# Optimization experiments

Measured on AMD Instinct MI355X. Metric: run time of the kernel, lower is better.

## Reference

```python
import jax, jax.numpy as jnp
import numpy as np
import math

# ---- config (matches init_kwargs / Mamba defaults) ----
B_SZ = 16
IMG = 224
PATCH = 16
D_MODEL = 384
DEPTH = 24
D_INNER = 2 * D_MODEL          # expand=2
D_STATE = 16
D_CONV = 4
DT_RANK = math.ceil(D_MODEL / D_STATE)
N_CLASSES = 1000
L_TOK = (IMG // PATCH) ** 2     # 196

C_CURV = 0.5
SQRT_C = math.sqrt(C_CURV)
MAX_NORM = 0.95 / SQRT_C

# ---- StablePoincareBall ops ----
def _norm(x):
    return jnp.sqrt(jnp.sum(x * x, axis=-1, keepdims=True) + 1e-15)

def expmap0(u):
    n = jnp.clip(_norm(u), 1e-8, 5.0)
    res = jnp.tanh(SQRT_C * n) / SQRT_C * (u / n)
    rn = _norm(res)
    scale = jnp.where(rn > MAX_NORM, MAX_NORM / rn, jnp.ones_like(rn))
    return res * scale

def logmap0(y):
    n = jnp.clip(_norm(y), 1e-8, MAX_NORM)
    return jnp.arctanh(jnp.minimum(SQRT_C * n, 0.95)) / SQRT_C * (y / n)

def mobius_add(a, b):
    xy = jnp.sum(a * b, -1, keepdims=True)
    x2 = jnp.sum(a * a, -1, keepdims=True)
    y2 = jnp.sum(b * b, -1, keepdims=True)
    num = (1 + 2 * C_CURV * xy + C_CURV * y2) * a + (1 - C_CURV * x2) * b
    den = 1 + 2 * C_CURV * xy + (C_CURV ** 2) * x2 * y2
    return num / jnp.maximum(den, 1e-15)

def mobius_matvec(M, x):
    xn = jnp.maximum(_norm(x), 1e-8)
    mx = x @ M.T
    mxn = jnp.maximum(_norm(mx), 1e-8)
    t = jnp.tanh(mxn / xn * jnp.arctanh(jnp.minimum(SQRT_C * xn, 1.0 - 1e-5)))
    return t * mx / (mxn * SQRT_C)

def hyp_layernorm(x, gamma, beta, eps=1e-5):
    t = logmap0(x)
    mean = t.mean(-1, keepdims=True)
    # torch .std() is unbiased (ddof=1)
    var = jnp.sum((t - mean) ** 2, -1, keepdims=True) / (t.shape[-1] - 1)
    tn = (t - mean) / (jnp.sqrt(var) + eps)
    return expmap0(tn * gamma + beta)

def silu(x):
    return x * jax.nn.sigmoid(x)

# ---- Mamba selective scan (recompute dA per step; carry only h) ----
def selective_scan(u, dt, A, Bm, Cm):
    # u, dt: (B,L,Din); A: (Din,N); Bm, Cm: (B,L,N)
    def step(h, inp):
        dt_t, B_t, C_t, u_t = inp              # (B,Din),(B,N),(B,N),(B,Din)
        dA = jnp.exp(dt_t[..., None] * A)      # (B,Din,N)
        h = dA * h + dt_t[..., None] * B_t[:, None, :] * u_t[..., None]
        y = jnp.sum(h * C_t[:, None, :], -1)   # (B,Din)
        return h, y
    h0 = jnp.zeros((u.shape[0], u.shape[2], A.shape[1]), u.dtype)
    _, ys = jax.lax.scan(step, h0, (dt.transpose(1, 0, 2), Bm.transpose(1, 0, 2),
                                    Cm.transpose(1, 0, 2), u.transpose(1, 0, 2)))
    return ys.transpose(1, 0, 2)               # (B,L,Din)

def mamba_mixer(x, in_w, cw, cb, xp_w, dt_w, dt_b, A_log, Dp, out_w):
    xz = x @ in_w.T                            # (B,L,2*Din)
    xc, z = xz[..., :D_INNER], xz[..., D_INNER:]
    xt = xc.transpose(0, 2, 1)                 # (B,Din,L)
    xpad = jnp.pad(xt, ((0, 0), (0, 0), (D_CONV - 1, 0)))
    L = xt.shape[-1]
    conv = sum(cw[:, k][None, :, None] * xpad[:, :, k:k + L] for k in range(D_CONV))
    conv = conv + cb[None, :, None]
    u = silu(conv.transpose(0, 2, 1))          # (B,L,Din)
    dbl = u @ xp_w.T                           # (B,L,dt_rank+2N)
    dt_r = dbl[..., :DT_RANK]
    Bm = dbl[..., DT_RANK:DT_RANK + D_STATE]
    Cm = dbl[..., DT_RANK + D_STATE:]
    dt = jax.nn.softplus(dt_r @ dt_w.T + dt_b)
    A = -jnp.exp(A_log)
    y = selective_scan(u, dt, A, Bm, Cm) + Dp * u
    y = y * silu(z)
    return y @ out_w.T


def setup_inputs() -> dict:
    key = jax.random.key(0)
    ks = jax.random.split(key, 24)
    f32 = jnp.float32
    inp = {}
    inp['x'] = jax.random.normal(ks[0], (B_SZ, 3, IMG, IMG), f32)
    inp['patch_w'] = jax.random.normal(ks[1], (D_MODEL, 3, PATCH, PATCH), f32) * 0.02
    inp['patch_b'] = jax.random.normal(ks[2], (D_MODEL,), f32) * 0.005
    inp['hyp_w'] = jax.random.normal(ks[3], (D_MODEL, D_MODEL), f32) * (1.0 / math.sqrt(D_MODEL))
    inp['hyp_b'] = jax.random.normal(ks[4], (D_MODEL,), f32) * 0.01
    inp['pe_gamma'] = jnp.ones((D_MODEL,), f32)
    inp['pe_beta'] = jnp.zeros((D_MODEL,), f32)
    inp['pos_embed'] = jax.random.normal(ks[5], (1, L_TOK, D_MODEL), f32) * 0.02
    inp['in_proj_w'] = jax.random.normal(ks[6], (DEPTH, 2 * D_INNER, D_MODEL), f32) * 0.02
    inp['conv_w'] = jax.random.normal(ks[7], (DEPTH, D_INNER, D_CONV), f32) * 0.1
    inp['conv_b'] = jnp.zeros((DEPTH, D_INNER), f32)
    inp['x_proj_w'] = jax.random.normal(ks[8], (DEPTH, DT_RANK + 2 * D_STATE, D_INNER), f32) * 0.02
    inp['dt_proj_w'] = jax.random.normal(ks[9], (DEPTH, D_INNER, DT_RANK), f32) * (1.0 / math.sqrt(DT_RANK))
    inp['dt_proj_b'] = jnp.log(jnp.expm1(jnp.full((DEPTH, D_INNER), 0.01, f32)))  # dt init ~0.01
    inp['A_log'] = jnp.tile(jnp.log(jnp.arange(1, D_STATE + 1, dtype=f32))[None, None, :], (DEPTH, D_INNER, 1))
    inp['Dp'] = jnp.ones((DEPTH, D_INNER), f32)
    inp['out_proj_w'] = jax.random.normal(ks[10], (DEPTH, D_MODEL, D_INNER), f32) * (0.02 / math.sqrt(DEPTH))
    inp['gamma'] = jnp.ones((DEPTH, D_MODEL), f32)
    inp['beta'] = jnp.zeros((DEPTH, D_MODEL), f32)
    inp['gamma_f'] = jnp.ones((D_MODEL,), f32)
    inp['beta_f'] = jnp.zeros((D_MODEL,), f32)
    inp['prototypes'] = expmap0(jax.random.normal(ks[11], (N_CLASSES, D_MODEL), f32) * 0.1)
    return inp


def reference(x, patch_w, patch_b, hyp_w, hyp_b, pe_gamma, pe_beta, pos_embed,
              in_proj_w, conv_w, conv_b, x_proj_w, dt_proj_w, dt_proj_b,
              A_log, Dp, out_proj_w, gamma, beta, gamma_f, beta_f, prototypes):
    # patch embed conv
    feat = jax.lax.conv_general_dilated(x, patch_w, (PATCH, PATCH), 'VALID',
                                        dimension_numbers=('NCHW', 'OIHW', 'NCHW'))
    feat = feat + patch_b[None, :, None, None]
    B, D, Hp, Wp = feat.shape
    tokens = feat.reshape(B, D, Hp * Wp).transpose(0, 2, 1)   # (B,L,D)
    h = expmap0(tokens)
    h = mobius_add(mobius_matvec(hyp_w, h), hyp_b)
    h = hyp_layernorm(h, pe_gamma, pe_beta)
    h = expmap0(logmap0(h) + pos_embed)                        # tangent-space pos add
    hidden, residual = h, None
    for i in range(DEPTH):
        residual = hidden if residual is None else hidden + residual
        hn = hyp_layernorm(residual, gamma[i], beta[i])
        hidden = mamba_mixer(hn, in_proj_w[i], conv_w[i], conv_b[i], x_proj_w[i],
                             dt_proj_w[i], dt_proj_b[i], A_log[i], Dp[i], out_proj_w[i])
    residual = hidden + residual
    hf = hyp_layernorm(residual, gamma_f, beta_f)
    pooled = expmap0(logmap0(hf).mean(axis=1))                 # tangent mean pool
    # hyperbolic distance head: logits = -dist(x, prototypes)
    diff = mobius_add(-pooled[:, None, :], prototypes[None])
    dn = jnp.minimum(SQRT_C * _norm(diff)[..., 0], 1.0 - 1e-5)
    return -(2.0 / SQRT_C) * jnp.arctanh(dn)                   # (B, num_classes)
```

## Files before the change

### kernel.cpp

```cpp
#include <hip/hip_runtime.h>
#include <hip/hip_bf16.h>
#include <math.h>

#define D_MODEL 384
#define D_INNER 768
#define D_STATE 16
#define DT_RANK 24
#define NXP 56
#define LTOK 196
#define BSZ 16
#define NROW 3136
#define NDEPTH 24
#define NCLS 1000

constexpr float kSqrtC   = 0.70710678118654752440f;
constexpr float kMaxNorm = 0.95f / 0.70710678118654752440f;

typedef unsigned short u16;
typedef short  bf16x8 __attribute__((ext_vector_type(8)));
typedef u16    u16x8  __attribute__((ext_vector_type(8)));
typedef float  f32x4  __attribute__((ext_vector_type(4)));

__device__ __forceinline__ float clampf(float x, float lo, float hi) {
  return fminf(fmaxf(x, lo), hi);
}

__device__ __forceinline__ u16 f2bf(float f) {
  union { float f; unsigned u; } v; v.f = f;
  return (u16)((v.u + 0x7FFFu + ((v.u >> 16) & 1u)) >> 16);
}
__device__ __forceinline__ float bf2f(u16 s) {
  union { unsigned u; float f; } v; v.u = ((unsigned)s) << 16;
  return v.f;
}

__device__ __forceinline__ void gload16(const u16* g, u16* l) {
  __builtin_amdgcn_global_load_lds(
      (const __attribute__((address_space(1))) unsigned int*)g,
      (__attribute__((address_space(3))) unsigned int*)l, 16, 0, 0);
}

__device__ __forceinline__ float fsig(float x) {
  return __fdividef(1.f, 1.f + __expf(-x));
}
__device__ __forceinline__ float fsilu(float x) { return x * fsig(x); }
__device__ __forceinline__ float fsoftplus(float x) {
  return (x > 20.f) ? x : __logf(1.f + __expf(x));
}
__device__ __forceinline__ float ftanh(float x) {
  float e = __expf(2.f * x);
  return __fdividef(e - 1.f, e + 1.f);
}
__device__ __forceinline__ float fatanh(float x) {
  return 0.5f * __logf(__fdividef(1.f + x, 1.f - x));
}

__device__ __forceinline__ float waveSum(float v) {
#pragma unroll
  for (int o = 1; o < 64; o <<= 1) v += __shfl_xor(v, o, 64);
  return v;
}

__device__ __forceinline__ float blockSum128(float v, float* sm) {
#pragma unroll
  for (int o = 32; o > 0; o >>= 1) v += __shfl_down(v, o, 64);
  __syncthreads();
  if ((threadIdx.x & 63) == 0) sm[threadIdx.x >> 6] = v;
  __syncthreads();
  return sm[0] + sm[1];
}

__global__ __launch_bounds__(256) void k_cvt(const float* __restrict__ s,
                                             u16* __restrict__ d, int n4) {
  int i = blockIdx.x * 256 + threadIdx.x;
  if (i >= n4) return;
  float4 v = ((const float4*)s)[i];
  short4 o = {(short)f2bf(v.x), (short)f2bf(v.y), (short)f2bf(v.z),
              (short)f2bf(v.w)};
  *(short4*)&d[(size_t)i * 4] = o;
}

__global__ __launch_bounds__(256) void k_im2col(const float* __restrict__ x,
                                                u16* __restrict__ P) {
  size_t idx = (size_t)blockIdx.x * 256 + threadIdx.x;
  if (idx >= (size_t)NROW * 768) return;
  int k = (int)(idx % 768);
  int r = (int)(idx / 768);
  int b = r / LTOK, t = r % LTOK;
  int hp = t / 14, wp = t % 14;
  int c = k / 256, rem = k % 256, i = rem / 16, j = rem % 16;
  P[idx] = f2bf(
      x[(((size_t)(b * 3 + c) * 224) + hp * 16 + i) * 224 + wp * 16 + j]);
}

__global__ __launch_bounds__(256) void k_gemm_bb(
    const u16* __restrict__ A, const u16* __restrict__ W,
    const float* __restrict__ bias, void* __restrict__ Cn,
    void* __restrict__ Ct, int K, int lda, int ldc, int ldct, int Nv, int act,
    int obf, int obf_t) {
  __shared__ u16 As[64 * 64];
  __shared__ u16 Ws[64 * 64];
  const int tid = threadIdx.x;
  const int m0 = blockIdx.x * 64;
  const int n0 = blockIdx.y * 64;
  const int lane = tid & 63;
  const int w = tid >> 6;
  const int wm = w & 1, wn = w >> 1;
  const int lm = lane & 15;
  const int quad = lane >> 4;
  const int r8 = lane >> 3;
  const int t8 = lane & 7;
  const int gsg = t8 ^ r8;
  const int s = lm & 7;

  f32x4 acc[2][2];
#pragma unroll
  for (int i = 0; i < 2; i++)
#pragma unroll
    for (int j = 0; j < 2; j++) acc[i][j] = (f32x4){0.f, 0.f, 0.f, 0.f};

  for (int k0 = 0; k0 < K; k0 += 64) {
    __syncthreads();
#pragma unroll
    for (int cc = 0; cc < 2; cc++) {
      const int c = 2 * w + cc;
      const int row = c * 8 + r8;
      gload16(A + (size_t)(m0 + row) * lda + k0 + gsg * 8,
              (u16*)As + (size_t)c * 512);
      gload16(W + (size_t)(n0 + row) * K + k0 + gsg * 8,
              (u16*)Ws + (size_t)c * 512);
    }
    __syncthreads();
#pragma unroll
    for (int h = 0; h < 2; h++) {
      const int col = (((h << 2) + quad) ^ s) << 3;
      bf16x8 af[2], bfr[2];
#pragma unroll
      for (int i = 0; i < 2; i++) {
        af[i]  = *(bf16x8*)&As[(wm * 32 + i * 16 + lm) * 64 + col];
        bfr[i] = *(bf16x8*)&Ws[(wn * 32 + i * 16 + lm) * 64 + col];
      }
#pragma unroll
      for (int i = 0; i < 2; i++)
#pragma unroll
        for (int j = 0; j < 2; j++)
          acc[i][j] = __builtin_amdgcn_mfma_f32_16x16x32_bf16(
              af[i], bfr[j], acc[i][j], 0, 0, 0);
    }
  }
#pragma unroll
  for (int i = 0; i < 2; i++) {
#pragma unroll
    for (int j = 0; j < 2; j++) {
      int cg = n0 + wn * 32 + j * 16 + lm;
      if (cg >= Nv) continue;
      float bj = bias ? bias[cg] : 0.f;
      float o[4];
      int rgb = m0 + wm * 32 + i * 16 + quad * 4;
#pragma unroll
      for (int reg = 0; reg < 4; reg++) {
        float v = acc[i][j][reg] + bj;
        if (act == 1) v = fsoftplus(v);
        else if (act == 2 && cg >= 768) v = fsilu(v);
        o[reg] = v;
      }
      if (Cn) {
#pragma unroll
        for (int reg = 0; reg < 4; reg++) {
          if (obf) ((u16*)Cn)[(size_t)(rgb + reg) * ldc + cg] = f2bf(o[reg]);
          else ((float*)Cn)[(size_t)(rgb + reg) * ldc + cg] = o[reg];
        }
      }
      if (Ct) {
        if (obf_t) {
          short4 o4 = {(short)f2bf(o[0]), (short)f2bf(o[1]), (short)f2bf(o[2]),
                       (short)f2bf(o[3])};
          *(short4*)&((u16*)Ct)[(size_t)cg * ldct + rgb] = o4;
        } else {
          float4 o4 = {o[0], o[1], o[2], o[3]};
          *(float4*)&((float*)Ct)[(size_t)cg * ldct + rgb] = o4;
        }
      }
    }
  }
}

__global__ __launch_bounds__(256) void k_gemm_n128(
    const u16* __restrict__ A, const u16* __restrict__ W,
    const float* __restrict__ bias, void* __restrict__ Cn, int K, int lda,
    int ldc, int act, int obf) {
  __shared__ u16 As[64 * 64];
  __shared__ u16 Ws[128 * 64];
  const int tid = threadIdx.x;
  const int m0 = blockIdx.x * 64;
  const int n0 = blockIdx.y * 128;
  const int lane = tid & 63;
  const int w = tid >> 6;
  const int lm = lane & 15;
  const int quad = lane >> 4;
  const int r8 = lane >> 3;
  const int t8 = lane & 7;
  const int gsg = t8 ^ r8;
  const int s = lm & 7;

  f32x4 acc[4][2];
#pragma unroll
  for (int i = 0; i < 4; i++)
#pragma unroll
    for (int j = 0; j < 2; j++) acc[i][j] = (f32x4){0.f, 0.f, 0.f, 0.f};

  for (int k0 = 0; k0 < K; k0 += 64) {
    __syncthreads();
#pragma unroll
    for (int cc = 0; cc < 2; cc++) {
      const int c = 2 * w + cc;
      gload16(A + (size_t)(m0 + c * 8 + r8) * lda + k0 + gsg * 8,
              (u16*)As + (size_t)c * 512);
    }
#pragma unroll
    for (int cc = 0; cc < 4; cc++) {
      const int c = 4 * w + cc;
      gload16(W + (size_t)(n0 + c * 8 + r8) * K + k0 + gsg * 8,
              (u16*)Ws + (size_t)c * 512);
    }
    __syncthreads();
#pragma unroll
    for (int h = 0; h < 2; h++) {
      const int col = (((h << 2) + quad) ^ s) << 3;
      bf16x8 af[4], bfr[2];
#pragma unroll
      for (int i = 0; i < 4; i++)
        af[i] = *(bf16x8*)&As[(i * 16 + lm) * 64 + col];
#pragma unroll
      for (int j = 0; j < 2; j++)
        bfr[j] = *(bf16x8*)&Ws[(w * 32 + j * 16 + lm) * 64 + col];
#pragma unroll
      for (int i = 0; i < 4; i++)
#pragma unroll
        for (int j = 0; j < 2; j++)
          acc[i][j] = __builtin_amdgcn_mfma_f32_16x16x32_bf16(
              af[i], bfr[j], acc[i][j], 0, 0, 0);
    }
  }
#pragma unroll
  for (int i = 0; i < 4; i++) {
#pragma unroll
    for (int j = 0; j < 2; j++) {
      int cg = n0 + w * 32 + j * 16 + lm;
      float bj = bias ? bias[cg] : 0.f;
      int rgb = m0 + i * 16 + quad * 4;
#pragma unroll
      for (int reg = 0; reg < 4; reg++) {
        float v = acc[i][j][reg] + bj;
        if (act == 1) v = fsoftplus(v);
        else if (act == 2 && cg >= 768) v = fsilu(v);
        if (obf) ((u16*)Cn)[(size_t)(rgb + reg) * ldc + cg] = f2bf(v);
        else ((float*)Cn)[(size_t)(rgb + reg) * ldc + cg] = v;
      }
    }
  }
}

__global__ __launch_bounds__(128) void k_stem_a(const float* __restrict__ tok,
                                                u16* __restrict__ hb,
                                                float* __restrict__ xn) {
  __shared__ float sm[2];
  const int r = blockIdx.x, tid = threadIdx.x;
  float v[3];
#pragma unroll
  for (int j = 0; j < 3; j++) v[j] = tok[(size_t)r * D_MODEL + tid + j * 128];
  float s = blockSum128(v[0] * v[0] + v[1] * v[1] + v[2] * v[2], sm);
  float n = sqrtf(s + 1e-15f);
  float nc = clampf(n, 1e-8f, 5.f);
  float ke = tanhf(kSqrtC * nc) / (kSqrtC * nc);
  float rn = sqrtf(ke * ke * s + 1e-15f);
  float sc = rn > kMaxNorm ? kMaxNorm / rn : 1.f;
  float kk = ke * sc;
#pragma unroll
  for (int j = 0; j < 3; j++)
    hb[(size_t)r * D_MODEL + tid + j * 128] = f2bf(kk * v[j]);
  if (tid == 0) xn[r] = fmaxf(sqrtf(kk * kk * s + 1e-15f), 1e-8f);
}

__global__ __launch_bounds__(128) void k_stem_b(
    const float* __restrict__ mx, const float* __restrict__ xn,
    const float* __restrict__ hyp_b, const float* __restrict__ pe_g,
    const float* __restrict__ pe_b, const float* __restrict__ pos,
    float* __restrict__ outh) {
  __shared__ float sm[2];
  const int r = blockIdx.x, tid = threadIdx.x;
  const int t = r % LTOK;
  float mv[3], bv[3];
  int dd[3];
#pragma unroll
  for (int j = 0; j < 3; j++) {
    dd[j] = tid + j * 128;
    mv[j] = mx[(size_t)r * D_MODEL + dd[j]];
    bv[j] = hyp_b[dd[j]];
  }
  float smx = blockSum128(mv[0] * mv[0] + mv[1] * mv[1] + mv[2] * mv[2], sm);
  float mxn = fmaxf(sqrtf(smx + 1e-15f), 1e-8f);
  float xnv = xn[r];
  float tt = tanhf(mxn / xnv * atanhf(fminf(kSqrtC * xnv, 1.f - 1e-5f)));
  float kres = tt / (mxn * kSqrtC);
  float res[3];
#pragma unroll
  for (int j = 0; j < 3; j++) res[j] = kres * mv[j];
  float xy = blockSum128(res[0] * bv[0] + res[1] * bv[1] + res[2] * bv[2], sm);
  float y2 = blockSum128(bv[0] * bv[0] + bv[1] * bv[1] + bv[2] * bv[2], sm);
  float x2 = kres * kres * smx;
  float al = 1.f + xy + 0.5f * y2;
  float be = 1.f - 0.5f * x2;
  float den = fmaxf(1.f + xy + 0.25f * x2 * y2, 1e-15f);
  float h1[3];
#pragma unroll
  for (int j = 0; j < 3; j++) h1[j] = (al * res[j] + be * bv[j]) / den;
  float s1 = blockSum128(h1[0] * h1[0] + h1[1] * h1[1] + h1[2] * h1[2], sm);
  float n1 = sqrtf(s1 + 1e-15f);
  float nc1 = clampf(n1, 1e-8f, kMaxNorm);
  float kl = atanhf(fminf(kSqrtC * nc1, 0.95f)) / (kSqrtC * nc1);
  float tl[3];
#pragma unroll
  for (int j = 0; j < 3; j++) tl[j] = kl * h1[j];
  float mean = blockSum128(tl[0] + tl[1] + tl[2], sm) * (1.f / 384.f);
  float dv = 0.f;
#pragma unroll
  for (int j = 0; j < 3; j++) { float d = tl[j] - mean; dv += d * d; }
  float var = blockSum128(dv, sm) * (1.f / 383.f);
  float inv = 1.f / (sqrtf(var) + 1e-5f);
  float g[3];
#pragma unroll
  for (int j = 0; j < 3; j++)
    g[j] = (tl[j] - mean) * inv * pe_g[dd[j]] + pe_b[dd[j]];
  float sg = blockSum128(g[0] * g[0] + g[1] * g[1] + g[2] * g[2], sm);
  float ng = sqrtf(sg + 1e-15f);
  float nc2 = clampf(ng, 1e-8f, 5.f);
  float ke = tanhf(kSqrtC * nc2) / (kSqrtC * nc2);
  float rn = sqrtf(ke * ke * sg + 1e-15f);
  float sc = rn > kMaxNorm ? kMaxNorm / rn : 1.f;
  float kk = ke * sc;
  float s2 = kk * kk * sg;
  float n3 = sqrtf(s2 + 1e-15f);
  float nc3 = clampf(n3, 1e-8f, kMaxNorm);
  float kl2 = atanhf(fminf(kSqrtC * nc3, 0.95f)) / (kSqrtC * nc3);
  float v[3];
#pragma unroll
  for (int j = 0; j < 3; j++)
    v[j] = kl2 * kk * g[j] + pos[(size_t)t * D_MODEL + dd[j]];
  float sv = blockSum128(v[0] * v[0] + v[1] * v[1] + v[2] * v[2], sm);
  float nv = sqrtf(sv + 1e-15f);
  float nc4 = clampf(nv, 1e-8f, 5.f);
  float ke2 = tanhf(kSqrtC * nc4) / (kSqrtC * nc4);
  float rn2 = sqrtf(ke2 * ke2 * sv + 1e-15f);
  float sc2 = rn2 > kMaxNorm ? kMaxNorm / rn2 : 1.f;
#pragma unroll
  for (int j = 0; j < 3; j++)
    outh[(size_t)r * D_MODEL + dd[j]] = ke2 * sc2 * v[j];
}

__global__ __launch_bounds__(256) void k_resln(
    const float* __restrict__ hid, const float* __restrict__ res_in,
    float* __restrict__ res_out, const float* __restrict__ g_,
    const float* __restrict__ b_, u16* __restrict__ out_bf,
    float* __restrict__ out_f, int first, int out_logmap) {
  const int lane = threadIdx.x & 63;
  const int r = blockIdx.x * 4 + (threadIdx.x >> 6);
  float v[6];
  int dd[6];
#pragma unroll
  for (int j = 0; j < 6; j++) {
    dd[j] = lane + j * 64;
    size_t idx = (size_t)r * D_MODEL + dd[j];
    v[j] = hid[idx] + (first ? 0.f : res_in[idx]);
    res_out[idx] = v[j];
  }
  float ss = 0.f;
#pragma unroll
  for (int j = 0; j < 6; j++) ss += v[j] * v[j];
  float s = waveSum(ss);
  float n = sqrtf(s + 1e-15f);
  float nc = clampf(n, 1e-8f, kMaxNorm);
  float kl = fatanh(fminf(kSqrtC * nc, 0.95f)) / (kSqrtC * nc);
  float t[6];
  float ts = 0.f;
#pragma unroll
  for (int j = 0; j < 6; j++) { t[j] = kl * v[j]; ts += t[j]; }
  float mean = waveSum(ts) * (1.f / 384.f);
  float dv = 0.f;
#pragma unroll
  for (int j = 0; j < 6; j++) { float d = t[j] - mean; dv += d * d; }
  float var = waveSum(dv) * (1.f / 383.f);
  float inv = 1.f / (sqrtf(var) + 1e-5f);
  float g[6];
  float gs = 0.f;
#pragma unroll
  for (int j = 0; j < 6; j++) {
    g[j] = (t[j] - mean) * inv * g_[dd[j]] + b_[dd[j]];
    gs += g[j] * g[j];
  }
  float sg = waveSum(gs);
  float ng = sqrtf(sg + 1e-15f);
  float nc2 = clampf(ng, 1e-8f, 5.f);
  float ke = ftanh(kSqrtC * nc2) / (kSqrtC * nc2);
  float rn = sqrtf(ke * ke * sg + 1e-15f);
  float sc = rn > kMaxNorm ? kMaxNorm / rn : 1.f;
  float kk = ke * sc;
  if (!out_logmap) {
#pragma unroll
    for (int j = 0; j < 6; j++)
      out_bf[(size_t)r * D_MODEL + dd[j]] = f2bf(kk * g[j]);
  } else {
    float s2 = kk * kk * sg;
    float n3 = sqrtf(s2 + 1e-15f);
    float nc3 = clampf(n3, 1e-8f, kMaxNorm);
    float kl2 = fatanh(fminf(kSqrtC * nc3, 0.95f)) / (kSqrtC * nc3);
#pragma unroll
    for (int j = 0; j < 6; j++)
      out_f[(size_t)r * D_MODEL + dd[j]] = kl2 * kk * g[j];
  }
}

__global__ __launch_bounds__(256) void k_convt(const u16* __restrict__ xz,
                                               const float* __restrict__ cw,
                                               const float* __restrict__ cb,
                                               u16* __restrict__ ut,
                                               u16* __restrict__ un) {
  __shared__ u16 sx[52][68];
  __shared__ u16 su2[49][68];
  const int d0 = blockIdx.x * 64;
  const int l0 = blockIdx.y * 49;
  const int b = blockIdx.z;
  const int t = threadIdx.x;
#pragma unroll
  for (int i = 0; i < 4; i++) {
    int idx = t + i * 256;
    if (idx < 832) {
      int row = idx >> 4, seg = idx & 15;
      int l = l0 - 3 + row;
      short4 v = {0, 0, 0, 0};
      if (l >= 0) {
        const u16* p = xz + (size_t)(b * LTOK + l) * (2 * D_INNER) + d0 + seg * 4;
        v = *(const short4*)p;
      }
      *(short4*)&sx[row][seg * 4] = v;
    }
  }
  __syncthreads();
  const int dl = t & 63, lg = t >> 6;
  const int d = d0 + dl;
  const float c0 = cw[d * 4], c1 = cw[d * 4 + 1], c2 = cw[d * 4 + 2],
              c3 = cw[d * 4 + 3];
  const float bb = cb[d];
  for (int l = lg; l < 49; l += 4) {
    float acc = bb;
    acc = fmaf(c0, bf2f(sx[l + 0][dl]), acc);
    acc = fmaf(c1, bf2f(sx[l + 1][dl]), acc);
    acc = fmaf(c2, bf2f(sx[l + 2][dl]), acc);
    acc = fmaf(c3, bf2f(sx[l + 3][dl]), acc);
    su2[l][dl] = f2bf(fsilu(acc));
  }
  __syncthreads();
#pragma unroll
  for (int i = 0; i < 13; i++) {
    int idx = t + i * 256;
    if (idx < 3136) {
      int d_ = idx / 49, l_ = idx % 49;
      ut[(size_t)(d0 + d_) * NROW + b * LTOK + l0 + l_] = su2[l_][d_];
    }
  }
#pragma unroll
  for (int i = 0; i < 13; i++) {
    int idx = t + i * 256;
    if (idx < 3136) {
      int l_ = idx >> 6, d_ = idx & 63;
      un[(size_t)(b * LTOK + l0 + l_) * D_INNER + d0 + d_] = su2[l_][d_];
    }
  }
}

__global__ __launch_bounds__(256) void k_pscan(
    const u16* __restrict__ ut, const float* __restrict__ dblt,
    const float* __restrict__ dt_w, const float* __restrict__ dt_bias,
    const float* __restrict__ A_log, const float* __restrict__ Dp,
    const u16* __restrict__ xz, u16* __restrict__ yf) {
  __shared__ float sdt[4][196];
  __shared__ float su[4][196];
  __shared__ float sprod[16][197];
  const int d0 = blockIdx.x * 4, b = blockIdx.y;
  const int t = threadIdx.x;
  const size_t col0 = (size_t)b * LTOK;
  short4 zq = {0, 0, 0, 0};
  if (t < 196) {
    float r[DT_RANK];
#pragma unroll
    for (int k = 0; k < DT_RANK; k++)
      r[k] = dblt[(size_t)k * NROW + col0 + t];
#pragma unroll
    for (int g = 0; g < 4; g++) {
      const int d = d0 + g;
      float acc = dt_bias[d];
#pragma unroll
      for (int k = 0; k < DT_RANK; k++)
        acc = fmaf(r[k], dt_w[d * DT_RANK + k], acc);
      sdt[g][t] = fsoftplus(acc);
      su[g][t] = bf2f(ut[(size_t)d * NROW + col0 + t]);
    }
    zq = *(const short4*)&xz[(col0 + t) * (2 * D_INNER) + D_INNER + d0];
  }
  const int c = t & 15, n = t >> 4;
  const bool act = c < 14;
  float Breg[14], Creg[14];
  if (act) {
    const float2* Bp =
        (const float2*)(dblt + (size_t)(DT_RANK + n) * NROW + col0 + c * 14);
    const float2* Cp = (const float2*)(
        dblt + (size_t)(DT_RANK + D_STATE + n) * NROW + col0 + c * 14);
#pragma unroll
    for (int j = 0; j < 7; j++) {
      float2 bv = Bp[j], cv = Cp[j];
      Breg[2 * j] = bv.x; Breg[2 * j + 1] = bv.y;
      Creg[2 * j] = cv.x; Creg[2 * j + 1] = cv.y;
    }
  }
  __syncthreads();
  u16 og[4];
  const u16 zz[4] = {(u16)zq.x, (u16)zq.y, (u16)zq.z, (u16)zq.w};
#pragma unroll
  for (int g = 0; g < 4; g++) {
    const int d = d0 + g;
    const float a = -__expf(A_log[(size_t)d * D_STATE + n]);
    float dA[14], hh[14];
    float A = 1.f, Bc = 0.f;
    if (act) {
      float h = 0.f, p = 1.f;
#pragma unroll
      for (int j = 0; j < 14; j++) {
        int l = c * 14 + j;
        float dtv = sdt[g][l];
        float e = __expf(dtv * a);
        h = fmaf(e, h, dtv * Breg[j] * su[g][l]);
        dA[j] = e;
        hh[j] = h;
        p *= e;
      }
      A = p;
      Bc = h;
    }
#pragma unroll
    for (int off = 1; off < 16; off <<= 1) {
      float pA = __shfl_up(A, off, 16);
      float pB = __shfl_up(Bc, off, 16);
      if (c >= off) {
        Bc = fmaf(A, pB, Bc);
        A *= pA;
      }
    }
    float h0 = __shfl_up(Bc, 1, 16);
    if (c == 0) h0 = 0.f;
    if (act) {
      float p = 1.f;
#pragma unroll
      for (int j = 0; j < 14; j++) {
        p *= dA[j];
        sprod[n][c * 14 + j] = fmaf(p, h0, hh[j]) * Creg[j];
      }
    }
    __syncthreads();
    if (t < 196) {
      float y = 0.f;
#pragma unroll
      for (int nn = 0; nn < 16; nn++) y += sprod[nn][t];
      float yv = bf2f(f2bf(fmaf(Dp[d], su[g][t], y)));
      og[g] = f2bf(yv * bf2f(zz[g]));
    }
    __syncthreads();
  }
  if (t < 196) {
    short4 o4 = {(short)og[0], (short)og[1], (short)og[2], (short)og[3]};
    *(short4*)&yf[(col0 + t) * D_INNER + d0] = o4;
  }
}

__global__ __launch_bounds__(128) void k_pool1(const float* __restrict__ tl,
                                               float* __restrict__ partial) {
  const int b = blockIdx.x, g = blockIdx.y, tid = threadIdx.x;
  float m[3] = {0.f, 0.f, 0.f};
  for (int l = g * 14; l < (g + 1) * 14; l++) {
    size_t row = ((size_t)b * LTOK + l) * D_MODEL;
#pragma unroll
    for (int j = 0; j < 3; j++) m[j] += tl[row + tid + j * 128];
  }
#pragma unroll
  for (int j = 0; j < 3; j++)
    partial[((size_t)b * 14 + g) * D_MODEL + tid + j * 128] = m[j];
}

__global__ __launch_bounds__(128) void k_pool2(const float* __restrict__ partial,
                                               float* __restrict__ pooled,
                                               float* __restrict__ x2v) {
  __shared__ float sm[2];
  const int b = blockIdx.x, tid = threadIdx.x;
  float m[3] = {0.f, 0.f, 0.f};
  for (int g = 0; g < 14; g++) {
    size_t row = ((size_t)b * 14 + g) * D_MODEL;
#pragma unroll
    for (int j = 0; j < 3; j++) m[j] += partial[row + tid + j * 128];
  }
#pragma unroll
  for (int j = 0; j < 3; j++) m[j] *= (1.f / (float)LTOK);
  float s = blockSum128(m[0] * m[0] + m[1] * m[1] + m[2] * m[2], sm);
  float n = sqrtf(s + 1e-15f);
  float nc = clampf(n, 1e-8f, 5.f);
  float ke = tanhf(kSqrtC * nc) / (kSqrtC * nc);
  float rn = sqrtf(ke * ke * s + 1e-15f);
  float sc = rn > kMaxNorm ? kMaxNorm / rn : 1.f;
  float kk = ke * sc;
  float p[3];
#pragma unroll
  for (int j = 0; j < 3; j++) {
    p[j] = kk * m[j];
    pooled[(size_t)b * D_MODEL + tid + j * 128] = p[j];
  }
  float s2 = blockSum128(p[0] * p[0] + p[1] * p[1] + p[2] * p[2], sm);
  if (tid == 0) x2v[b] = s2;
}

__global__ __launch_bounds__(256) void k_head(const float* __restrict__ pooled,
                                              const float* __restrict__ protos,
                                              const float* __restrict__ x2v,
                                              float* __restrict__ out) {
  __shared__ float sp[D_MODEL];
  const int b = blockIdx.y;
  const int c = blockIdx.x * 256 + threadIdx.x;
  for (int j = threadIdx.x; j < D_MODEL; j += 256)
    sp[j] = pooled[(size_t)b * D_MODEL + j];
  __syncthreads();
  if (c >= NCLS) return;
  const float* pr = protos + (size_t)c * D_MODEL;
  float dotv = 0.f, y2 = 0.f;
  for (int k = 0; k < D_MODEL; k++) {
    float w = pr[k];
    dotv += sp[k] * w;
    y2 += w * w;
  }
  float x2 = x2v[b];
  float xy = -dotv;
  float al = 1.f + xy + 0.5f * y2;
  float be = 1.f - 0.5f * x2;
  float num2 = al * al * x2 + 2.f * al * be * xy + be * be * y2;
  float den = fmaxf(1.f + xy + 0.25f * x2 * y2, 1e-15f);
  float r2 = num2 / (den * den) + 1e-15f;
  float dn = fminf(kSqrtC * sqrtf(r2), 1.f - 1e-5f);
  out[(size_t)b * NCLS + c] = -(2.f / kSqrtC) * atanhf(dn);
}

extern "C" void kernel_launch(void* const* d_in, const int* in_sizes, int n_in,
                              void* d_out, int out_size, void* d_ws,
                              size_t ws_size, hipStream_t stream) {
  const float* x        = (const float*)d_in[0];
  const float* patch_w  = (const float*)d_in[1];
  const float* patch_b  = (const float*)d_in[2];
  const float* hyp_w    = (const float*)d_in[3];
  const float* hyp_b    = (const float*)d_in[4];
  const float* pe_gamma = (const float*)d_in[5];
  const float* pe_beta  = (const float*)d_in[6];
  const float* pos      = (const float*)d_in[7];
  const float* in_w     = (const float*)d_in[8];
  const float* conv_w   = (const float*)d_in[9];
  const float* conv_b   = (const float*)d_in[10];
  const float* xp_w     = (const float*)d_in[11];
  const float* dt_w     = (const float*)d_in[12];
  const float* dt_bias  = (const float*)d_in[13];
  const float* A_log    = (const float*)d_in[14];
  const float* Dp       = (const float*)d_in[15];
  const float* out_w    = (const float*)d_in[16];
  const float* gamma    = (const float*)d_in[17];
  const float* beta     = (const float*)d_in[18];
  const float* gamma_f  = (const float*)d_in[19];
  const float* beta_f   = (const float*)d_in[20];
  const float* protos   = (const float*)d_in[21];
  float* out = (float*)d_out;

  char* cur = (char*)d_ws;
  auto alloc = [&](size_t bytes) {
    char* p = cur;
    cur += (bytes + 255) & ~(size_t)255;
    return (void*)p;
  };
  float* hidden  = (float*)alloc((size_t)NROW * D_MODEL * 4);
  float* resid   = (float*)alloc((size_t)NROW * D_MODEL * 4);
  float* dblt    = (float*)alloc((size_t)64 * NROW * 4);
  float* fscr    = (float*)alloc((size_t)NROW * 768 * 4);
  float* xn      = (float*)alloc((size_t)NROW * 4);
  float* pooled  = (float*)alloc((size_t)BSZ * D_MODEL * 4);
  float* x2v     = (float*)alloc((size_t)BSZ * 4);
  float* partial = (float*)alloc((size_t)BSZ * 14 * D_MODEL * 4);
  u16* hn_bf  = (u16*)alloc((size_t)NROW * D_MODEL * 2);
  u16* xz_bf  = (u16*)alloc((size_t)NROW * 2 * D_INNER * 2);
  u16* ut     = (u16*)alloc((size_t)D_INNER * NROW * 2);
  u16* u_bf   = (u16*)alloc((size_t)NROW * D_INNER * 2);
  u16* yf     = (u16*)alloc((size_t)NROW * D_INNER * 2);
  const size_t n_inw  = (size_t)NDEPTH * 2 * D_INNER * D_MODEL;
  const size_t n_outw = (size_t)NDEPTH * D_MODEL * D_INNER;
  const size_t n_xpw  = (size_t)NDEPTH * NXP * D_INNER;
  const size_t n_pw   = (size_t)D_MODEL * 768;
  const size_t n_hw   = (size_t)D_MODEL * D_MODEL;
  u16* in_wb  = (u16*)alloc(n_inw * 2);
  u16* out_wb = (u16*)alloc(n_outw * 2);
  u16* xp_wb  = (u16*)alloc(n_xpw * 2);
  u16* p_wb   = (u16*)alloc(n_pw * 2);
  u16* h_wb   = (u16*)alloc(n_hw * 2);
  u16* P_bf     = ut;
  float* tokens = fscr;
  float* mx     = fscr + (size_t)NROW * D_MODEL;
  float* hnf    = fscr;

  k_cvt<<<dim3((int)((n_inw / 4 + 255) / 256)), dim3(256), 0, stream>>>(
      in_w, in_wb, (int)(n_inw / 4));
  k_cvt<<<dim3((int)((n_outw / 4 + 255) / 256)), dim3(256), 0, stream>>>(
      out_w, out_wb, (int)(n_outw / 4));
  k_cvt<<<dim3((int)((n_xpw / 4 + 255) / 256)), dim3(256), 0, stream>>>(
      xp_w, xp_wb, (int)(n_xpw / 4));
  k_cvt<<<dim3((int)((n_pw / 4 + 255) / 256)), dim3(256), 0, stream>>>(
      patch_w, p_wb, (int)(n_pw / 4));
  k_cvt<<<dim3((int)((n_hw / 4 + 255) / 256)), dim3(256), 0, stream>>>(
      hyp_w, h_wb, (int)(n_hw / 4));

  k_im2col<<<dim3((NROW * 768) / 256), dim3(256), 0, stream>>>(x, P_bf);
  k_gemm_bb<<<dim3(NROW / 64, 6), dim3(256), 0, stream>>>(
      P_bf, p_wb, patch_b, tokens, nullptr, 768, 768, D_MODEL, 0, D_MODEL, 0,
      0, 0);
  k_stem_a<<<dim3(NROW), dim3(128), 0, stream>>>(tokens, hn_bf, xn);
  k_gemm_bb<<<dim3(NROW / 64, 6), dim3(256), 0, stream>>>(
      hn_bf, h_wb, nullptr, mx, nullptr, D_MODEL, D_MODEL, D_MODEL, 0, D_MODEL,
      0, 0, 0);
  k_stem_b<<<dim3(NROW), dim3(128), 0, stream>>>(mx, xn, hyp_b, pe_gamma,
                                                 pe_beta, pos, hidden);
  for (int i = 0; i < NDEPTH; i++) {
    k_resln<<<dim3(NROW / 4), dim3(256), 0, stream>>>(
        hidden, resid, resid, gamma + (size_t)i * D_MODEL,
        beta + (size_t)i * D_MODEL, hn_bf, nullptr, i == 0 ? 1 : 0, 0);
    k_gemm_n128<<<dim3(NROW / 64, (2 * D_INNER) / 128), dim3(256), 0, stream>>>(
        hn_bf, in_wb + (size_t)i * 2 * D_INNER * D_MODEL, nullptr, xz_bf,
        D_MODEL, D_MODEL, 2 * D_INNER, 2, 1);
    k_convt<<<dim3(12, 4, BSZ), dim3(256), 0, stream>>>(
        xz_bf, conv_w + (size_t)i * D_INNER * 4, conv_b + (size_t)i * D_INNER,
        ut, u_bf);
    k_gemm_bb<<<dim3(NROW / 64, 1), dim3(256), 0, stream>>>(
        u_bf, xp_wb + (size_t)i * NXP * D_INNER, nullptr, nullptr, dblt,
        D_INNER, D_INNER, 0, NROW, NXP, 0, 0, 0);
    k_pscan<<<dim3(D_INNER / 4, BSZ), dim3(256), 0, stream>>>(
        ut, dblt, dt_w + (size_t)i * D_INNER * DT_RANK,
        dt_bias + (size_t)i * D_INNER, A_log + (size_t)i * D_INNER * D_STATE,
        Dp + (size_t)i * D_INNER, xz_bf, yf);
    k_gemm_bb<<<dim3(NROW / 64, 6), dim3(256), 0, stream>>>(
        yf, out_wb + (size_t)i * D_MODEL * D_INNER, nullptr, hidden, nullptr,
        D_INNER, D_INNER, D_MODEL, 0, D_MODEL, 0, 0, 0);
  }
  k_resln<<<dim3(NROW / 4), dim3(256), 0, stream>>>(
      hidden, resid, resid, gamma_f, beta_f, nullptr, hnf, 0, 1);
  k_pool1<<<dim3(BSZ, 14), dim3(128), 0, stream>>>(hnf, partial);
  k_pool2<<<dim3(BSZ), dim3(128), 0, stream>>>(partial, pooled, x2v);
  k_head<<<dim3((NCLS + 255) / 256, BSZ), dim3(256), 0, stream>>>(pooled,
                                                                  protos, x2v,
                                                                  out);
}
```

Measured before the change: 2.211 ms.

## Double-buffer GEMM shared-memory tiles and merge weight conversion launches

Both bf16 GEMM kernels now use two shared-memory buffers. The next K tile is loaded while MFMAs run on the current one, and only one barrier is left per iteration. The five per-tensor fp32-to-bf16 weight conversion kernels are merged into one launch that picks source and destination by index range. Shared memory per block doubles, which can lower occupancy. The prefetch overlap depends on gload16 being asynchronous or the compiler scheduling it early.

Result: no change. 2.169 ms (-1.9%).

```diff
diff --git a/kernel.cpp b/kernel.cpp
--- a/kernel.cpp
+++ b/kernel.cpp
@@ -70,10 +70,20 @@
   return sm[0] + sm[1];
 }
 
-__global__ __launch_bounds__(256) void k_cvt(const float* __restrict__ s,
-                                             u16* __restrict__ d, int n4) {
+__global__ __launch_bounds__(256) void k_cvt5(
+    const float* __restrict__ s0, u16* __restrict__ d0, int n0,
+    const float* __restrict__ s1, u16* __restrict__ d1, int n1,
+    const float* __restrict__ s2, u16* __restrict__ d2, int n2,
+    const float* __restrict__ s3, u16* __restrict__ d3, int n3,
+    const float* __restrict__ s4, u16* __restrict__ d4, int n4) {
   int i = blockIdx.x * 256 + threadIdx.x;
-  if (i >= n4) return;
+  const float* s; u16* d;
+  if (i < n0) { s = s0; d = d0; }
+  else if ((i -= n0) < n1) { s = s1; d = d1; }
+  else if ((i -= n1) < n2) { s = s2; d = d2; }
+  else if ((i -= n2) < n3) { s = s3; d = d3; }
+  else if ((i -= n3) < n4) { s = s4; d = d4; }
+  else return;
   float4 v = ((const float4*)s)[i];
   short4 o = {(short)f2bf(v.x), (short)f2bf(v.y), (short)f2bf(v.z),
               (short)f2bf(v.w)};
@@ -98,8 +108,8 @@
     const float* __restrict__ bias, void* __restrict__ Cn,
     void* __restrict__ Ct, int K, int lda, int ldc, int ldct, int Nv, int act,
     int obf, int obf_t) {
-  __shared__ u16 As[64 * 64];
-  __shared__ u16 Ws[64 * 64];
+  __shared__ u16 As[2][64 * 64];
+  __shared__ u16 Ws[2][64 * 64];
   const int tid = threadIdx.x;
   const int m0 = blockIdx.x * 64;
   const int n0 = blockIdx.y * 64;
@@ -119,26 +129,30 @@
 #pragma unroll
     for (int j = 0; j < 2; j++) acc[i][j] = (f32x4){0.f, 0.f, 0.f, 0.f};
 
-  for (int k0 = 0; k0 < K; k0 += 64) {
-    __syncthreads();
+  const u16* rowA = A + (size_t)(m0 + (2 * w) * 8 + r8) * lda;
+  auto stage = [&](int buf, int k0) {
 #pragma unroll
     for (int cc = 0; cc < 2; cc++) {
       const int c = 2 * w + cc;
       const int row = c * 8 + r8;
-      gload16(A + (size_t)(m0 + row) * lda + k0 + gsg * 8,
-              (u16*)As + (size_t)c * 512);
-      gload16(W + (size_t)(n0 + row) * K + k0 + gsg * 8,
-              (u16*)Ws + (size_t)c * 512);
-    }
-    __syncthreads();
+      gload16(A + (size_t)(m0 + row) * lda + k0 + gsg * 8, &As[buf][c * 512]);
+      gload16(W + (size_t)(n0 + row) * K + k0 + gsg * 8, &Ws[buf][c * 512]);
+    }
+  };
+  (void)rowA;
+  stage(0, 0);
+  __syncthreads();
+  int cur = 0;
+  for (int k0 = 0; k0 < K; k0 += 64) {
+    if (k0 + 64 < K) stage(cur ^ 1, k0 + 64);
 #pragma unroll
     for (int h = 0; h < 2; h++) {
       const int col = (((h << 2) + quad) ^ s) << 3;
       bf16x8 af[2], bfr[2];
 #pragma unroll
       for (int i = 0; i < 2; i++) {
-        af[i]  = *(bf16x8*)&As[(wm * 32 + i * 16 + lm) * 64 + col];
-        bfr[i] = *(bf16x8*)&Ws[(wn * 32 + i * 16 + lm) * 64 + col];
+        af[i]  = *(bf16x8*)&As[cur][(wm * 32 + i * 16 + lm) * 64 + col];
+        bfr[i] = *(bf16x8*)&Ws[cur][(wn * 32 + i * 16 + lm) * 64 + col];
       }
 #pragma unroll
       for (int i = 0; i < 2; i++)
@@ -147,6 +161,8 @@
           acc[i][j] = __builtin_amdgcn_mfma_f32_16x16x32_bf16(
               af[i], bfr[j], acc[i][j], 0, 0, 0);
     }
+    __syncthreads();
+    cur ^= 1;
   }
 #pragma unroll
   for (int i = 0; i < 2; i++) {
@@ -189,8 +205,8 @@
     const u16* __restrict__ A, const u16* __restrict__ W,
     const float* __restrict__ bias, void* __restrict__ Cn, int K, int lda,
     int ldc, int act, int obf) {
-  __shared__ u16 As[64 * 64];
-  __shared__ u16 Ws[128 * 64];
+  __shared__ u16 As[2][64 * 64];
+  __shared__ u16 Ws[2][128 * 64];
   const int tid = threadIdx.x;
   const int m0 = blockIdx.x * 64;
   const int n0 = blockIdx.y * 128;
@@ -209,31 +225,35 @@
 #pragma unroll
     for (int j = 0; j < 2; j++) acc[i][j] = (f32x4){0.f, 0.f, 0.f, 0.f};
 
-  for (int k0 = 0; k0 < K; k0 += 64) {
-    __syncthreads();
+  auto stage = [&](int buf, int k0) {
 #pragma unroll
     for (int cc = 0; cc < 2; cc++) {
       const int c = 2 * w + cc;
       gload16(A + (size_t)(m0 + c * 8 + r8) * lda + k0 + gsg * 8,
-              (u16*)As + (size_t)c * 512);
+              &As[buf][c * 512]);
     }
 #pragma unroll
     for (int cc = 0; cc < 4; cc++) {
       const int c = 4 * w + cc;
       gload16(W + (size_t)(n0 + c * 8 + r8) * K + k0 + gsg * 8,
-              (u16*)Ws + (size_t)c * 512);
-    }
-    __syncthreads();
+              &Ws[buf][c * 512]);
+    }
+  };
+  stage(0, 0);
+  __syncthreads();
+  int cur = 0;
+  for (int k0 = 0; k0 < K; k0 += 64) {
+    if (k0 + 64 < K) stage(cur ^ 1, k0 + 64);
 #pragma unroll
     for (int h = 0; h < 2; h++) {
       const int col = (((h << 2) + quad) ^ s) << 3;
       bf16x8 af[4], bfr[2];
 #pragma unroll
       for (int i = 0; i < 4; i++)
-        af[i] = *(bf16x8*)&As[(i * 16 + lm) * 64 + col];
+        af[i] = *(bf16x8*)&As[cur][(i * 16 + lm) * 64 + col];
 #pragma unroll
       for (int j = 0; j < 2; j++)
-        bfr[j] = *(bf16x8*)&Ws[(w * 32 + j * 16 + lm) * 64 + col];
+        bfr[j] = *(bf16x8*)&Ws[cur][(w * 32 + j * 16 + lm) * 64 + col];
 #pragma unroll
       for (int i = 0; i < 4; i++)
 #pragma unroll
@@ -241,6 +261,8 @@
           acc[i][j] = __builtin_amdgcn_mfma_f32_16x16x32_bf16(
               af[i], bfr[j], acc[i][j], 0, 0, 0);
     }
+    __syncthreads();
+    cur ^= 1;
   }
 #pragma unroll
   for (int i = 0; i < 4; i++) {
@@ -715,16 +737,15 @@
   float* mx     = fscr + (size_t)NROW * D_MODEL;
   float* hnf    = fscr;
 
-  k_cvt<<<dim3((int)((n_inw / 4 + 255) / 256)), dim3(256), 0, stream>>>(
-      in_w, in_wb, (int)(n_inw / 4));
-  k_cvt<<<dim3((int)((n_outw / 4 + 255) / 256)), dim3(256), 0, stream>>>(
-      out_w, out_wb, (int)(n_outw / 4));
-  k_cvt<<<dim3((int)((n_xpw / 4 + 255) / 256)), dim3(256), 0, stream>>>(
-      xp_w, xp_wb, (int)(n_xpw / 4));
-  k_cvt<<<dim3((int)((n_pw / 4 + 255) / 256)), dim3(256), 0, stream>>>(
-      patch_w, p_wb, (int)(n_pw / 4));
-  k_cvt<<<dim3((int)((n_hw / 4 + 255) / 256)), dim3(256), 0, stream>>>(
-      hyp_w, h_wb, (int)(n_hw / 4));
+  {
+    const int c0 = (int)(n_inw / 4), c1 = (int)(n_outw / 4),
+              c2 = (int)(n_xpw / 4), c3 = (int)(n_pw / 4),
+              c4 = (int)(n_hw / 4);
+    const int tot = c0 + c1 + c2 + c3 + c4;
+    k_cvt5<<<dim3((tot + 255) / 256), dim3(256), 0, stream>>>(
+        in_w, in_wb, c0, out_w, out_wb, c1, xp_w, xp_wb, c2, patch_w, p_wb,
+        c3, hyp_w, h_wb, c4);
+  }
 
   k_im2col<<<dim3((NROW * 768) / 256), dim3(256), 0, stream>>>(x, P_bf);
   k_gemm_bb<<<dim3(NROW / 64, 6), dim3(256), 0, stream>>>(
```
